# Optimization experiments

Measured on AMD Instinct MI355X. Metric: run time of the kernel, lower is better.

Reference implementation:

```python
import jax, jax.numpy as jnp
import numpy as np

VOCAB, HDIM, NC = 32000, 256, 5
B, L = 256, 512  # L must be a power of 2 (complete binary tree, depth log2(L))


def setup_inputs() -> dict:
    key = jax.random.key(0)
    ks = jax.random.split(key, 8)
    s_e = 1.0 / np.sqrt(HDIM)
    s_r = 1.0 / np.sqrt(2 * HDIM)
    return {
        "tokens": jax.random.randint(ks[0], (B, L), 0, VOCAB),                        # leaf word ids
        "embed_table": jax.random.normal(ks[1], (VOCAB, HDIM), jnp.float32),          # nn.Embedding
        "WR_w": jax.random.uniform(ks[2], (HDIM, 2 * HDIM), jnp.float32, -s_r, s_r),  # Linear(2H->H)
        "WR_b": jax.random.uniform(ks[3], (HDIM,), jnp.float32, -s_r, s_r),
        "WF_w": jax.random.uniform(ks[4], (HDIM, HDIM), jnp.float32, -s_e, s_e),      # Linear(H->H)
        "WF_b": jax.random.uniform(ks[5], (HDIM,), jnp.float32, -s_e, s_e),
        "WO_w": jax.random.uniform(ks[6], (NC, HDIM), jnp.float32, -s_e, s_e),        # Linear(H->NC)
        "WO_b": jax.random.uniform(ks[7], (NC,), jnp.float32, -s_e, s_e),
    }


def reference(tokens, embed_table, WR_w, WR_b, WF_w, WF_b, WO_w, WO_b):
    # Leaves: embedding gather. [B, L, H]
    e = embed_table[tokens]
    # Batched-by-depth tree composition: tanh(WR(cat(left, right))) per level.
    # Loop is over log2(L) levels (static), fully vectorized within each level.
    while e.shape[1] > 1:
        cat = jnp.concatenate([e[:, 0::2], e[:, 1::2]], axis=-1)   # [B, n/2, 2H]
        e = jnp.tanh(jnp.einsum('bnd,hd->bnh', cat, WR_w) + WR_b)  # [B, n/2, H]
    root = e[:, 0]  # [B, H]
    # classify: WO(ReLU(WF(root)))
    hidden = jax.nn.relu(root @ WF_w.T + WF_b)
    return hidden @ WO_w.T + WO_b  # [B, NC] logits
```

## Files before the change

kernel.cpp:

```cpp
#include <hip/hip_runtime.h>
#include <hip/hip_bf16.h>

typedef __bf16 bf16_t;
typedef __bf16 bf16x8 __attribute__((ext_vector_type(8)));
typedef __bf16 bf16x4 __attribute__((ext_vector_type(4)));
typedef float f32x4 __attribute__((ext_vector_type(4)));

__device__ __forceinline__ bf16_t f2bf(float f) {
    __hip_bfloat16 h = __float2bfloat16(f);
    return __builtin_bit_cast(bf16_t, h);
}

__device__ __forceinline__ float tanh_fast(float s) {
    float e2x = __expf(2.0f * s);
    return 1.0f - 2.0f * __builtin_amdgcn_rcpf(e2x + 1.0f);
}

__device__ __forceinline__ int swz(int u) { return u ^ ((u >> 3) & 7); }

#define GLD16(g, l)                                                        \
    __builtin_amdgcn_global_load_lds(                                      \
        (const __attribute__((address_space(1))) void*)(g),                \
        (__attribute__((address_space(3))) void*)(l), 16, 0, 0)

#define WAITV4() asm volatile("s_waitcnt vmcnt(4)" ::: "memory")
#define WAITV0() asm volatile("s_waitcnt vmcnt(0)" ::: "memory")

__global__ void __launch_bounds__(256) setup_kernel(const float* __restrict__ table,
                                                    const float* __restrict__ WRw,
                                                    bf16_t* __restrict__ tableBf,
                                                    bf16_t* __restrict__ Wbf,
                                                    bf16_t* __restrict__ Wfrag) {
    const int b = blockIdx.x, tid = threadIdx.x;
    if (b < 8000) {
        int i = b * 256 + tid;
        float4 v = ((const float4*)table)[i];
        bf16x4 o;
        o[0] = f2bf(v.x); o[1] = f2bf(v.y); o[2] = f2bf(v.z); o[3] = f2bf(v.w);
        ((bf16x4*)tableBf)[i] = o;
    } else if (b < 8128) {
        int i = (b - 8000) * 256 + tid;
        float4 v = ((const float4*)WRw)[i];
        bf16x4 o;
        o[0] = f2bf(v.x); o[1] = f2bf(v.y); o[2] = f2bf(v.z); o[3] = f2bf(v.w);
        ((bf16x4*)Wbf)[i] = o;
    } else {
        int gt = (b - 8128) * 256 + tid;
        int n16 = gt >> 10, rem = gt & 1023;
        int kt = rem >> 6, ln = rem & 63;
        int r = n16 * 16 + (ln & 15);
        int c = kt * 32 + (ln >> 4) * 8;
        const float4* s = (const float4*)(WRw + (long)r * 512 + c);
        float4 v0 = s[0], v1 = s[1];
        bf16x8 o;
        o[0] = f2bf(v0.x); o[1] = f2bf(v0.y); o[2] = f2bf(v0.z); o[3] = f2bf(v0.w);
        o[4] = f2bf(v1.x); o[5] = f2bf(v1.y); o[6] = f2bf(v1.z); o[7] = f2bf(v1.w);
        *(bf16x8*)(Wfrag + (size_t)gt * 8) = o;
    }
}

template <bool GATHER>
__global__ void __launch_bounds__(256) level_gemm(const bf16_t* __restrict__ A,
                                                  const int* __restrict__ tokens,
                                                  const bf16_t* __restrict__ tableBf,
                                                  const bf16_t* __restrict__ W,
                                                  const float* __restrict__ bias,
                                                  bf16_t* __restrict__ out) {
    constexpr int K = 512, N = 256;
    __shared__ __align__(16) char lds[49152];

    const int tid = threadIdx.x;
    const int lane = tid & 63;
    const int w = tid >> 6;
    const int wm = w >> 1, wn = w & 1;
    const long brow = (long)blockIdx.x * 128;
    const int bcol = blockIdx.y * 128;
    const int lr = lane & 15;
    const int g = lane >> 4;

    const int vlin = (w << 6) | lane;
    const int vs = swz(vlin);
    const int srow = vs >> 2;
    const int scolE = (vs & 3) << 3;

    const bf16_t *paLo0, *paHi0, *paLo1, *paHi1, *pa0, *pa1;
    if constexpr (GATHER) {
        long m0 = brow + srow, m1 = m0 + 64;
        int t0a = tokens[2 * m0], t0b = tokens[2 * m0 + 1];
        int t1a = tokens[2 * m1], t1b = tokens[2 * m1 + 1];
        paLo0 = tableBf + (long)t0a * 256 + scolE;
        paHi0 = tableBf + (long)t0b * 256 + scolE;
        paLo1 = tableBf + (long)t1a * 256 + scolE;
        paHi1 = tableBf + (long)t1b * 256 + scolE;
    } else {
        pa0 = A + (brow + srow) * K + scolE;
        pa1 = A + (brow + srow + 64) * K + scolE;
    }
    const bf16_t* pw0 = W + (long)(bcol + srow) * K + scolE;
    const bf16_t* pw1 = pw0 + 64 * K;

    float bv[4];
#pragma unroll
    for (int nt = 0; nt < 4; ++nt)
        bv[nt] = bias[bcol + (wn << 6) + (nt << 4) + lr];

    int offA[4], offB[4];
#pragma unroll
    for (int mt = 0; mt < 4; ++mt) {
        int rowA = (wm << 6) + (mt << 4) + lr;
        offA[mt] = swz(rowA * 4 + g) * 16;
    }
#pragma unroll
    for (int nt = 0; nt < 4; ++nt) {
        int rowB = (wn << 6) + (nt << 4) + lr;
        offB[nt] = 8192 + swz(rowB * 4 + g) * 16;
    }

    auto stage = [&](int buf, int kt) {
        char* dA = lds + buf * 16384 + (w << 10);
        char* dB = dA + 8192;
        const bf16_t *s0, *s1;
        if constexpr (GATHER) {
            int klo = kt & 255;
            bool lo = kt < 256;
            s0 = (lo ? paLo0 : paHi0) + klo;
            s1 = (lo ? paLo1 : paHi1) + klo;
        } else {
            s0 = pa0 + kt;
            s1 = pa1 + kt;
        }
        GLD16(s0, dA);
        GLD16(s1, dA + 4096);
        GLD16(pw0 + kt, dB);
        GLD16(pw1 + kt, dB + 4096);
    };

    f32x4 acc[4][4];
    const f32x4 zero = {0.f, 0.f, 0.f, 0.f};
#pragma unroll
    for (int i = 0; i < 4; ++i)
#pragma unroll
        for (int j = 0; j < 4; ++j) acc[i][j] = zero;

    stage(0, 0);
    stage(1, 32);
    WAITV4();
    __builtin_amdgcn_s_barrier();

#pragma unroll
    for (int t = 0; t < 16; ++t) {
        const int bufOff = 16384 * (t % 3);
        if (t + 2 < 16) stage((t + 2) % 3, (t + 2) << 5);

        bf16x8 af[4], bfr[4];
#pragma unroll
        for (int mt = 0; mt < 4; ++mt)
            af[mt] = *(const bf16x8*)(lds + bufOff + offA[mt]);
#pragma unroll
        for (int nt = 0; nt < 4; ++nt)
            bfr[nt] = *(const bf16x8*)(lds + bufOff + offB[nt]);
#pragma unroll
        for (int mt = 0; mt < 4; ++mt)
#pragma unroll
            for (int nt = 0; nt < 4; ++nt)
                acc[mt][nt] = __builtin_amdgcn_mfma_f32_16x16x32_bf16(
                    af[mt], bfr[nt], acc[mt][nt], 0, 0, 0);

        if (t < 14) {
            WAITV4();
            __builtin_amdgcn_s_barrier();
        } else if (t == 14) {
            WAITV0();
            __builtin_amdgcn_s_barrier();
        }
    }

    const int crow = g << 2;
#pragma unroll
    for (int nt = 0; nt < 4; ++nt) {
        int col = bcol + (wn << 6) + (nt << 4) + lr;
#pragma unroll
        for (int mt = 0; mt < 4; ++mt) {
            long row0 = brow + (wm << 6) + (mt << 4) + crow;
#pragma unroll
            for (int r = 0; r < 4; ++r)
                out[(row0 + r) * N + col] = f2bf(tanh_fast(acc[mt][nt][r] + bv[nt]));
        }
    }
}

__device__ __forceinline__ void tail_level(const char* chIn, char* chOut,
                                           const bf16_t* __restrict__ wfBase,
                                           const float* bv, int lane) {
    const int lr = lane & 15;
    const int g = lane >> 4;
    const char* aBase = chIn + lr * 1040 + g * 16;

    f32x4 acc[4];
    const f32x4 zero = {0.f, 0.f, 0.f, 0.f};
#pragma unroll
    for (int nt = 0; nt < 4; ++nt) acc[nt] = zero;

#pragma unroll
    for (int kt = 0; kt < 16; ++kt) {
        bf16x8 af = *(const bf16x8*)(aBase + kt * 64);
#pragma unroll
        for (int nt = 0; nt < 4; ++nt) {
            bf16x8 bfv = *(const bf16x8*)(wfBase + ((nt << 4) + kt) * 512);
            acc[nt] = __builtin_amdgcn_mfma_f32_16x16x32_bf16(af, bfv, acc[nt], 0, 0, 0);
        }
    }

    const int crow = g << 2;
#pragma unroll
    for (int nt = 0; nt < 4; ++nt) {
#pragma unroll
        for (int r = 0; r < 4; ++r) {
            int R = crow + r;
            float vv = tanh_fast(acc[nt][r] + bv[nt]);
            ((void)0);
        }
    }
}

__device__ __forceinline__ void tail_level_w(const char* chIn, char* chOut,
                                             const bf16_t* __restrict__ wfBase,
                                             const float* bv, int w, int lane) {
    const int lr = lane & 15;
    const int g = lane >> 4;
    const char* aBase = chIn + lr * 1040 + g * 16;

    f32x4 acc[4];
    const f32x4 zero = {0.f, 0.f, 0.f, 0.f};
#pragma unroll
    for (int nt = 0; nt < 4; ++nt) acc[nt] = zero;

#pragma unroll
    for (int kt = 0; kt < 16; ++kt) {
        bf16x8 af = *(const bf16x8*)(aBase + kt * 64);
#pragma unroll
        for (int nt = 0; nt < 4; ++nt) {
            bf16x8 bfv = *(const bf16x8*)(wfBase + ((nt << 4) + kt) * 512);
            acc[nt] = __builtin_amdgcn_mfma_f32_16x16x32_bf16(af, bfv, acc[nt], 0, 0, 0);
        }
    }

    const int crow = g << 2;
#pragma unroll
    for (int nt = 0; nt < 4; ++nt) {
        int col = (w << 6) + (nt << 4) + lr;
#pragma unroll
        for (int r = 0; r < 4; ++r) {
            int R = crow + r;
            float vv = tanh_fast(acc[nt][r] + bv[nt]);
            *(bf16_t*)(chOut + (R >> 1) * 1040 + (((R & 1) << 8) + col) * 2) = f2bf(vv);
        }
    }
}

__global__ void __launch_bounds__(256) tail_kernel(const bf16_t* __restrict__ in,
                                                   const bf16_t* __restrict__ Wfrag,
                                                   const float* __restrict__ bias,
                                                   const float* __restrict__ WFw,
                                                   const float* __restrict__ WFb,
                                                   const float* __restrict__ WOw,
                                                   const float* __restrict__ WOb,
                                                   float* __restrict__ out) {
    __shared__ __align__(16) char tl[2][16640];
    __shared__ float hid[256];

    const int tid = threadIdx.x;
    const int lane = tid & 63;
    const int w = tid >> 6;
    const int lr = lane & 15;

    float bv[4];
#pragma unroll
    for (int nt = 0; nt < 4; ++nt) bv[nt] = bias[(w << 6) + (nt << 4) + lr];

    const bf16_t* wfBase = Wfrag + ((size_t)((w << 2) << 4) << 6) * 8 / 8;
    wfBase = Wfrag + (size_t)(((w << 2) * 16) * 64 + lane) * 8;

    const bf16_t* gin = in + (size_t)blockIdx.x * 8192;
#pragma unroll
    for (int j = 0; j < 4; ++j) {
        int i = j * 256 + tid;
        int4 v = *(const int4*)(gin + i * 8);
        *(int4*)(&tl[0][0] + (i >> 6) * 1040 + (i & 63) * 16) = v;
    }
    __syncthreads();

    tail_level_w(tl[0], tl[1], wfBase, bv, w, lane);  __syncthreads();
    tail_level_w(tl[1], tl[0], wfBase, bv, w, lane);  __syncthreads();
    tail_level_w(tl[0], tl[1], wfBase, bv, w, lane);  __syncthreads();
    tail_level_w(tl[1], tl[0], wfBase, bv, w, lane);  __syncthreads();
    tail_level_w(tl[0], tl[1], wfBase, bv, w, lane);  __syncthreads();

    const bf16_t* root = (const bf16_t*)&tl[1][0];
    float s = WFb[tid];
    const float4* wf = (const float4*)(WFw + (long)tid * 256);
#pragma unroll 8
    for (int k4 = 0; k4 < 64; ++k4) {
        float4 wv = wf[k4];
        int k = k4 << 2;
        bf16x4 rv = *(const bf16x4*)&root[k];
        s += (float)rv[0] * wv.x + (float)rv[1] * wv.y +
             (float)rv[2] * wv.z + (float)rv[3] * wv.w;
    }
    hid[tid] = fmaxf(s, 0.0f);
    __syncthreads();

    if (tid < 5) {
        float o = WOb[tid];
        const float* wo = WOw + tid * 256;
        for (int k = 0; k < 256; ++k) o += hid[k] * wo[k];
        out[(long)blockIdx.x * 5 + tid] = o;
    }
}

extern "C" void kernel_launch(void* const* d_in, const int* in_sizes, int n_in,
                              void* d_out, int out_size, void* d_ws, size_t ws_size,
                              hipStream_t stream) {
    const int*   tokens = (const int*)d_in[0];
    const float* table  = (const float*)d_in[1];
    const float* WRw    = (const float*)d_in[2];
    const float* WRb    = (const float*)d_in[3];
    const float* WFw    = (const float*)d_in[4];
    const float* WFb    = (const float*)d_in[5];
    const float* WOw    = (const float*)d_in[6];
    const float* WOb    = (const float*)d_in[7];
    float* out = (float*)d_out;

    char* ws = (char*)d_ws;
    bf16_t* tableBf = (bf16_t*)ws;
    bf16_t* Wbf   = (bf16_t*)(ws + (size_t)20971520);
    bf16_t* Wfrag = (bf16_t*)(ws + (size_t)22020096);
    bf16_t* buf0  = (bf16_t*)(ws + (size_t)25165824);
    bf16_t* buf1  = (bf16_t*)(ws + (size_t)67108864);

    setup_kernel<<<8192, 256, 0, stream>>>(table, WRw, tableBf, Wbf, Wfrag);

    level_gemm<true><<<dim3(512, 2), 256, 0, stream>>>(nullptr, tokens, tableBf,
                                                       Wbf, WRb, buf0);
    level_gemm<false><<<dim3(256, 2), 256, 0, stream>>>(buf0, nullptr, nullptr,
                                                        Wbf, WRb, buf1);
    level_gemm<false><<<dim3(128, 2), 256, 0, stream>>>(buf1, nullptr, nullptr,
                                                        Wbf, WRb, buf0);
    level_gemm<false><<<dim3(64, 2), 256, 0, stream>>>(buf0, nullptr, nullptr,
                                                       Wbf, WRb, buf1);
    tail_kernel<<<256, 256, 0, stream>>>(buf1, Wfrag, WRb, WFw, WFb, WOw, WOb, out);
}
```

Baseline: 188.6 us.

## Fuse tree levels 2-9 and classifier into one per-sample LDS-resident kernel

Replaces the four per-level GEMM launches plus the tail kernel with two kernels. The first is a level-1 gather GEMM using 512-thread blocks that cover all 256 output columns. The second is a per-sample tree kernel that computes levels 2 through 9 entirely in LDS using a swizzled activation buffer. This removes the global round-trips of intermediate activations and the extra launches. It also transposes WF in setup for coalesced classifier reads and does the final WO projection with a shuffle reduction. In exchange it uses only 256 blocks with large LDS footprints, so occupancy and parallelism in the later levels are limited.

```diff
diff --git a/kernel.cpp b/kernel.cpp
--- a/kernel.cpp
+++ b/kernel.cpp
@@ -17,20 +17,27 @@
 }
 
 __device__ __forceinline__ int swz(int u) { return u ^ ((u >> 3) & 7); }
+__device__ __forceinline__ int actswz(int a) {
+    return a ^ ((((a >> 10) ^ (a >> 13)) & 7) << 4);
+}
 
 #define GLD16(g, l)                                                        \
     __builtin_amdgcn_global_load_lds(                                      \
         (const __attribute__((address_space(1))) void*)(g),                \
         (__attribute__((address_space(3))) void*)(l), 16, 0, 0)
 
-#define WAITV4() asm volatile("s_waitcnt vmcnt(4)" ::: "memory")
+#define WAITV3() asm volatile("s_waitcnt vmcnt(3)" ::: "memory")
+#define WAITV2() asm volatile("s_waitcnt vmcnt(2)" ::: "memory")
 #define WAITV0() asm volatile("s_waitcnt vmcnt(0)" ::: "memory")
+#define BAR() __builtin_amdgcn_s_barrier()
 
 __global__ void __launch_bounds__(256) setup_kernel(const float* __restrict__ table,
                                                     const float* __restrict__ WRw,
+                                                    const float* __restrict__ WFw,
                                                     bf16_t* __restrict__ tableBf,
                                                     bf16_t* __restrict__ Wbf,
-                                                    bf16_t* __restrict__ Wfrag) {
+                                                    bf16_t* __restrict__ Wfrag,
+                                                    float* __restrict__ WFwT) {
     const int b = blockIdx.x, tid = threadIdx.x;
     if (b < 8000) {
         int i = b * 256 + tid;
@@ -44,7 +51,7 @@
         bf16x4 o;
         o[0] = f2bf(v.x); o[1] = f2bf(v.y); o[2] = f2bf(v.z); o[3] = f2bf(v.w);
         ((bf16x4*)Wbf)[i] = o;
-    } else {
+    } else if (b < 8192) {
         int gt = (b - 8128) * 256 + tid;
         int n16 = gt >> 10, rem = gt & 1023;
         int kt = rem >> 6, ln = rem & 63;
@@ -56,83 +63,57 @@
         o[0] = f2bf(v0.x); o[1] = f2bf(v0.y); o[2] = f2bf(v0.z); o[3] = f2bf(v0.w);
         o[4] = f2bf(v1.x); o[5] = f2bf(v1.y); o[6] = f2bf(v1.z); o[7] = f2bf(v1.w);
         *(bf16x8*)(Wfrag + (size_t)gt * 8) = o;
-    }
-}
-
-template <bool GATHER>
-__global__ void __launch_bounds__(256) level_gemm(const bf16_t* __restrict__ A,
-                                                  const int* __restrict__ tokens,
-                                                  const bf16_t* __restrict__ tableBf,
-                                                  const bf16_t* __restrict__ W,
-                                                  const float* __restrict__ bias,
-                                                  bf16_t* __restrict__ out) {
-    constexpr int K = 512, N = 256;
-    __shared__ __align__(16) char lds[49152];
-
-    const int tid = threadIdx.x;
-    const int lane = tid & 63;
-    const int w = tid >> 6;
-    const int wm = w >> 1, wn = w & 1;
+    } else {
+        int i0 = (b - 8192) * 1024 + tid * 4;
+        float4 v;
+        v.x = WFw[((i0 + 0) & 255) * 256 + ((i0 + 0) >> 8)];
+        v.y = WFw[((i0 + 1) & 255) * 256 + ((i0 + 1) >> 8)];
+        v.z = WFw[((i0 + 2) & 255) * 256 + ((i0 + 2) >> 8)];
+        v.w = WFw[((i0 + 3) & 255) * 256 + ((i0 + 3) >> 8)];
+        *(float4*)(WFwT + i0) = v;
+    }
+}
+
+__global__ void __launch_bounds__(512) l1_kernel(const int* __restrict__ tokens,
+                                                 const bf16_t* __restrict__ tableBf,
+                                                 const bf16_t* __restrict__ W,
+                                                 const float* __restrict__ bias,
+                                                 bf16_t* __restrict__ out) {
+    __shared__ __align__(16) char lds[73728];
+    const int tid = threadIdx.x, lane = tid & 63, w = tid >> 6;
+    const int wm = w >> 2, wn = w & 3, lr = lane & 15, g = lane >> 4;
     const long brow = (long)blockIdx.x * 128;
-    const int bcol = blockIdx.y * 128;
-    const int lr = lane & 15;
-    const int g = lane >> 4;
-
-    const int vlin = (w << 6) | lane;
-    const int vs = swz(vlin);
-    const int srow = vs >> 2;
-    const int scolE = (vs & 3) << 3;
-
-    const bf16_t *paLo0, *paHi0, *paLo1, *paHi1, *pa0, *pa1;
-    if constexpr (GATHER) {
-        long m0 = brow + srow, m1 = m0 + 64;
-        int t0a = tokens[2 * m0], t0b = tokens[2 * m0 + 1];
-        int t1a = tokens[2 * m1], t1b = tokens[2 * m1 + 1];
-        paLo0 = tableBf + (long)t0a * 256 + scolE;
-        paHi0 = tableBf + (long)t0b * 256 + scolE;
-        paLo1 = tableBf + (long)t1a * 256 + scolE;
-        paHi1 = tableBf + (long)t1b * 256 + scolE;
-    } else {
-        pa0 = A + (brow + srow) * K + scolE;
-        pa1 = A + (brow + srow + 64) * K + scolE;
-    }
-    const bf16_t* pw0 = W + (long)(bcol + srow) * K + scolE;
-    const bf16_t* pw1 = pw0 + 64 * K;
+
+    const int ua = (w << 6) + swz(lane);
+    const int arow = ua >> 2, acolE = (ua & 3) << 3;
+    const long m = brow + arow;
+    const int tokA = tokens[2 * m], tokB = tokens[2 * m + 1];
+    const bf16_t* paLo = tableBf + (long)tokA * 256 + acolE;
+    const bf16_t* paHi = tableBf + (long)tokB * 256 + acolE;
+
+    const int ub0 = (w << 6) + swz(lane);
+    const int ub1 = ((w + 8) << 6) + swz(lane);
+    const bf16_t* pb0 = W + (long)(ub0 >> 2) * 512 + ((ub0 & 3) << 3);
+    const bf16_t* pb1 = W + (long)(ub1 >> 2) * 512 + ((ub1 & 3) << 3);
 
     float bv[4];
 #pragma unroll
+    for (int nt = 0; nt < 4; ++nt) bv[nt] = bias[(wn << 6) + (nt << 4) + lr];
+
+    int offA[4], offB[4];
+#pragma unroll
+    for (int mt = 0; mt < 4; ++mt)
+        offA[mt] = swz((((wm << 6) + (mt << 4) + lr) << 2) + g) << 4;
+#pragma unroll
     for (int nt = 0; nt < 4; ++nt)
-        bv[nt] = bias[bcol + (wn << 6) + (nt << 4) + lr];
-
-    int offA[4], offB[4];
-#pragma unroll
-    for (int mt = 0; mt < 4; ++mt) {
-        int rowA = (wm << 6) + (mt << 4) + lr;
-        offA[mt] = swz(rowA * 4 + g) * 16;
-    }
-#pragma unroll
-    for (int nt = 0; nt < 4; ++nt) {
-        int rowB = (wn << 6) + (nt << 4) + lr;
-        offB[nt] = 8192 + swz(rowB * 4 + g) * 16;
-    }
-
-    auto stage = [&](int buf, int kt) {
-        char* dA = lds + buf * 16384 + (w << 10);
-        char* dB = dA + 8192;
-        const bf16_t *s0, *s1;
-        if constexpr (GATHER) {
-            int klo = kt & 255;
-            bool lo = kt < 256;
-            s0 = (lo ? paLo0 : paHi0) + klo;
-            s1 = (lo ? paLo1 : paHi1) + klo;
-        } else {
-            s0 = pa0 + kt;
-            s1 = pa1 + kt;
-        }
-        GLD16(s0, dA);
-        GLD16(s1, dA + 4096);
-        GLD16(pw0 + kt, dB);
-        GLD16(pw1 + kt, dB + 4096);
+        offB[nt] = 8192 + (swz((((wn << 6) + (nt << 4) + lr) << 2) + g) << 4);
+
+    auto stage = [&](int s, int kt) {
+        char* base = lds + s * 24576;
+        bool lo = kt < 256;
+        GLD16((lo ? paLo : paHi) + (kt & 255), base + (w << 10));
+        GLD16(pb0 + kt, base + 8192 + (w << 10));
+        GLD16(pb1 + kt, base + 8192 + ((w + 8) << 10));
     };
 
     f32x4 acc[4][4];
@@ -144,177 +125,291 @@
 
     stage(0, 0);
     stage(1, 32);
-    WAITV4();
-    __builtin_amdgcn_s_barrier();
+    WAITV3(); BAR();
 
 #pragma unroll
     for (int t = 0; t < 16; ++t) {
-        const int bufOff = 16384 * (t % 3);
+        const char* base = lds + (t % 3) * 24576;
         if (t + 2 < 16) stage((t + 2) % 3, (t + 2) << 5);
-
         bf16x8 af[4], bfr[4];
 #pragma unroll
-        for (int mt = 0; mt < 4; ++mt)
-            af[mt] = *(const bf16x8*)(lds + bufOff + offA[mt]);
-#pragma unroll
-        for (int nt = 0; nt < 4; ++nt)
-            bfr[nt] = *(const bf16x8*)(lds + bufOff + offB[nt]);
+        for (int mt = 0; mt < 4; ++mt) af[mt] = *(const bf16x8*)(base + offA[mt]);
+#pragma unroll
+        for (int nt = 0; nt < 4; ++nt) bfr[nt] = *(const bf16x8*)(base + offB[nt]);
 #pragma unroll
         for (int mt = 0; mt < 4; ++mt)
 #pragma unroll
             for (int nt = 0; nt < 4; ++nt)
                 acc[mt][nt] = __builtin_amdgcn_mfma_f32_16x16x32_bf16(
                     af[mt], bfr[nt], acc[mt][nt], 0, 0, 0);
-
-        if (t < 14) {
-            WAITV4();
-            __builtin_amdgcn_s_barrier();
-        } else if (t == 14) {
-            WAITV0();
-            __builtin_amdgcn_s_barrier();
-        }
+        if (t < 14)      { WAITV3(); BAR(); }
+        else if (t == 14){ WAITV0(); BAR(); }
     }
 
     const int crow = g << 2;
 #pragma unroll
     for (int nt = 0; nt < 4; ++nt) {
-        int col = bcol + (wn << 6) + (nt << 4) + lr;
+        int col = (wn << 6) + (nt << 4) + lr;
 #pragma unroll
         for (int mt = 0; mt < 4; ++mt) {
             long row0 = brow + (wm << 6) + (mt << 4) + crow;
 #pragma unroll
             for (int r = 0; r < 4; ++r)
-                out[(row0 + r) * N + col] = f2bf(tanh_fast(acc[mt][nt][r] + bv[nt]));
-        }
-    }
-}
-
-__device__ __forceinline__ void tail_level(const char* chIn, char* chOut,
-                                           const bf16_t* __restrict__ wfBase,
-                                           const float* bv, int lane) {
-    const int lr = lane & 15;
-    const int g = lane >> 4;
-    const char* aBase = chIn + lr * 1040 + g * 16;
-
-    f32x4 acc[4];
-    const f32x4 zero = {0.f, 0.f, 0.f, 0.f};
-#pragma unroll
-    for (int nt = 0; nt < 4; ++nt) acc[nt] = zero;
-
-#pragma unroll
-    for (int kt = 0; kt < 16; ++kt) {
-        bf16x8 af = *(const bf16x8*)(aBase + kt * 64);
-#pragma unroll
-        for (int nt = 0; nt < 4; ++nt) {
-            bf16x8 bfv = *(const bf16x8*)(wfBase + ((nt << 4) + kt) * 512);
-            acc[nt] = __builtin_amdgcn_mfma_f32_16x16x32_bf16(af, bfv, acc[nt], 0, 0, 0);
-        }
-    }
-
-    const int crow = g << 2;
-#pragma unroll
-    for (int nt = 0; nt < 4; ++nt) {
-#pragma unroll
-        for (int r = 0; r < 4; ++r) {
-            int R = crow + r;
-            float vv = tanh_fast(acc[nt][r] + bv[nt]);
-            ((void)0);
-        }
-    }
-}
-
-__device__ __forceinline__ void tail_level_w(const char* chIn, char* chOut,
-                                             const bf16_t* __restrict__ wfBase,
-                                             const float* bv, int w, int lane) {
-    const int lr = lane & 15;
-    const int g = lane >> 4;
-    const char* aBase = chIn + lr * 1040 + g * 16;
-
-    f32x4 acc[4];
-    const f32x4 zero = {0.f, 0.f, 0.f, 0.f};
-#pragma unroll
-    for (int nt = 0; nt < 4; ++nt) acc[nt] = zero;
-
-#pragma unroll
-    for (int kt = 0; kt < 16; ++kt) {
-        bf16x8 af = *(const bf16x8*)(aBase + kt * 64);
-#pragma unroll
-        for (int nt = 0; nt < 4; ++nt) {
-            bf16x8 bfv = *(const bf16x8*)(wfBase + ((nt << 4) + kt) * 512);
-            acc[nt] = __builtin_amdgcn_mfma_f32_16x16x32_bf16(af, bfv, acc[nt], 0, 0, 0);
-        }
-    }
-
-    const int crow = g << 2;
-#pragma unroll
-    for (int nt = 0; nt < 4; ++nt) {
-        int col = (w << 6) + (nt << 4) + lr;
-#pragma unroll
-        for (int r = 0; r < 4; ++r) {
-            int R = crow + r;
-            float vv = tanh_fast(acc[nt][r] + bv[nt]);
-            *(bf16_t*)(chOut + (R >> 1) * 1040 + (((R & 1) << 8) + col) * 2) = f2bf(vv);
-        }
-    }
-}
-
-__global__ void __launch_bounds__(256) tail_kernel(const bf16_t* __restrict__ in,
+                out[(row0 + r) * 256 + col] = f2bf(tanh_fast(acc[mt][nt][r] + bv[nt]));
+        }
+    }
+}
+
+__global__ void __launch_bounds__(512) tree_kernel(const bf16_t* __restrict__ l1out,
+                                                   const bf16_t* __restrict__ W,
                                                    const bf16_t* __restrict__ Wfrag,
                                                    const float* __restrict__ bias,
-                                                   const float* __restrict__ WFw,
+                                                   const float* __restrict__ WFwT,
                                                    const float* __restrict__ WFb,
                                                    const float* __restrict__ WOw,
                                                    const float* __restrict__ WOb,
                                                    float* __restrict__ out) {
-    __shared__ __align__(16) char tl[2][16640];
+    __shared__ __align__(16) char stg[73728];
+    __shared__ __align__(16) char act[65536];
     __shared__ float hid[256];
 
-    const int tid = threadIdx.x;
-    const int lane = tid & 63;
-    const int w = tid >> 6;
-    const int lr = lane & 15;
+    const int tid = threadIdx.x, lane = tid & 63, w = tid >> 6;
+    const int wm = w >> 2, wn = w & 3, lr = lane & 15, g = lane >> 4;
+    const int crow = g << 2;
+    const bf16_t* Abase = l1out + (size_t)blockIdx.x * 65536;
+
+    const int ua = (w << 6) + swz(lane);
+    const bf16_t* pa = Abase + (long)(ua >> 2) * 512 + ((ua & 3) << 3);
+    const int ub0 = (w << 6) + swz(lane);
+    const int ub1 = ((w + 8) << 6) + swz(lane);
+    const bf16_t* pb0 = W + (long)(ub0 >> 2) * 512 + ((ub0 & 3) << 3);
+    const bf16_t* pb1 = W + (long)(ub1 >> 2) * 512 + ((ub1 & 3) << 3);
 
     float bv[4];
 #pragma unroll
-    for (int nt = 0; nt < 4; ++nt) bv[nt] = bias[(w << 6) + (nt << 4) + lr];
-
-    const bf16_t* wfBase = Wfrag + ((size_t)((w << 2) << 4) << 6) * 8 / 8;
-    wfBase = Wfrag + (size_t)(((w << 2) * 16) * 64 + lane) * 8;
-
-    const bf16_t* gin = in + (size_t)blockIdx.x * 8192;
-#pragma unroll
-    for (int j = 0; j < 4; ++j) {
-        int i = j * 256 + tid;
-        int4 v = *(const int4*)(gin + i * 8);
-        *(int4*)(&tl[0][0] + (i >> 6) * 1040 + (i & 63) * 16) = v;
+    for (int nt = 0; nt < 4; ++nt) bv[nt] = bias[(wn << 6) + (nt << 4) + lr];
+    float bvT[2];
+#pragma unroll
+    for (int nt = 0; nt < 2; ++nt) bvT[nt] = bias[(w << 5) + (nt << 4) + lr];
+
+    int offB[4];
+#pragma unroll
+    for (int nt = 0; nt < 4; ++nt)
+        offB[nt] = swz((((wn << 6) + (nt << 4) + lr) << 2) + g) << 4;
+
+    {
+        int offA[4];
+#pragma unroll
+        for (int mt = 0; mt < 4; ++mt)
+            offA[mt] = swz((((wm << 6) + (mt << 4) + lr) << 2) + g) << 4;
+
+        auto stage = [&](int s, int kt) {
+            char* base = stg + s * 24576;
+            GLD16(pa + kt, base + (w << 10));
+            GLD16(pb0 + kt, base + 8192 + (w << 10));
+            GLD16(pb1 + kt, base + 8192 + ((w + 8) << 10));
+        };
+
+        f32x4 acc[4][4];
+        const f32x4 zero = {0.f, 0.f, 0.f, 0.f};
+#pragma unroll
+        for (int i = 0; i < 4; ++i)
+#pragma unroll
+            for (int j = 0; j < 4; ++j) acc[i][j] = zero;
+
+        stage(0, 0); stage(1, 32);
+        WAITV3(); BAR();
+#pragma unroll
+        for (int t = 0; t < 16; ++t) {
+            const char* base = stg + (t % 3) * 24576;
+            if (t + 2 < 16) stage((t + 2) % 3, (t + 2) << 5);
+            bf16x8 af[4], bfr[4];
+#pragma unroll
+            for (int mt = 0; mt < 4; ++mt) af[mt] = *(const bf16x8*)(base + 8192 * 0 + offA[mt]);
+#pragma unroll
+            for (int nt = 0; nt < 4; ++nt) bfr[nt] = *(const bf16x8*)(base + 8192 + offB[nt]);
+#pragma unroll
+            for (int mt = 0; mt < 4; ++mt)
+#pragma unroll
+                for (int nt = 0; nt < 4; ++nt)
+                    acc[mt][nt] = __builtin_amdgcn_mfma_f32_16x16x32_bf16(
+                        af[mt], bfr[nt], acc[mt][nt], 0, 0, 0);
+            if (t < 14)      { WAITV3(); BAR(); }
+            else if (t == 14){ WAITV0(); BAR(); }
+        }
+#pragma unroll
+        for (int nt = 0; nt < 4; ++nt) {
+            int col = (wn << 6) + (nt << 4) + lr;
+#pragma unroll
+            for (int mt = 0; mt < 4; ++mt) {
+                int m0 = (wm << 6) + (mt << 4) + crow;
+#pragma unroll
+                for (int r = 0; r < 4; ++r) {
+                    int a = ((m0 + r) << 9) + (col << 1);
+                    *(bf16_t*)(act + actswz(a)) = f2bf(tanh_fast(acc[mt][nt][r] + bv[nt]));
+                }
+            }
+        }
+        __syncthreads();
+    }
+
+    {
+        auto stageB = [&](int s, int kt) {
+            char* base = stg + s * 16384;
+            GLD16(pb0 + kt, base + (w << 10));
+            GLD16(pb1 + kt, base + ((w + 8) << 10));
+        };
+        f32x4 acc[2][4];
+        const f32x4 zero = {0.f, 0.f, 0.f, 0.f};
+#pragma unroll
+        for (int i = 0; i < 2; ++i)
+#pragma unroll
+            for (int j = 0; j < 4; ++j) acc[i][j] = zero;
+
+        stageB(0, 0); stageB(1, 32);
+        WAITV2(); BAR();
+#pragma unroll
+        for (int t = 0; t < 16; ++t) {
+            const char* base = stg + (t % 3) * 16384;
+            if (t + 2 < 16) stageB((t + 2) % 3, (t + 2) << 5);
+            bf16x8 af[2], bfr[4];
+#pragma unroll
+            for (int mt = 0; mt < 2; ++mt) {
+                int row = (wm << 5) + (mt << 4) + lr;
+                int a = (row << 10) + (t << 6) + (g << 4);
+                af[mt] = *(const bf16x8*)(act + actswz(a));
+            }
+#pragma unroll
+            for (int nt = 0; nt < 4; ++nt) bfr[nt] = *(const bf16x8*)(base + offB[nt]);
+#pragma unroll
+            for (int mt = 0; mt < 2; ++mt)
+#pragma unroll
+                for (int nt = 0; nt < 4; ++nt)
+                    acc[mt][nt] = __builtin_amdgcn_mfma_f32_16x16x32_bf16(
+                        af[mt], bfr[nt], acc[mt][nt], 0, 0, 0);
+            if (t < 14)      { WAITV2(); BAR(); }
+            else if (t == 14){ WAITV0(); BAR(); }
+        }
+        __syncthreads();
+#pragma unroll
+        for (int nt = 0; nt < 4; ++nt) {
+            int col = (wn << 6) + (nt << 4) + lr;
+#pragma unroll
+            for (int mt = 0; mt < 2; ++mt) {
+                int m0 = (wm << 5) + (mt << 4) + crow;
+#pragma unroll
+                for (int r = 0; r < 4; ++r) {
+                    int a = ((m0 + r) << 10) + (col << 1);
+                    *(bf16_t*)(act + actswz(a)) = f2bf(tanh_fast(acc[mt][nt][r] + bv[nt]));
+                }
+            }
+        }
+        __syncthreads();
+    }
+
+    {
+        auto stageB = [&](int s, int kt) {
+            char* base = stg + s * 16384;
+            GLD16(pb0 + kt, base + (w << 10));
+            GLD16(pb1 + kt, base + ((w + 8) << 10));
+        };
+        f32x4 acc[4];
+        const f32x4 zero = {0.f, 0.f, 0.f, 0.f};
+#pragma unroll
+        for (int j = 0; j < 4; ++j) acc[j] = zero;
+
+        stageB(0, 0); stageB(1, 32);
+        WAITV2(); BAR();
+#pragma unroll
+        for (int t = 0; t < 16; ++t) {
+            const char* base = stg + (t % 3) * 16384;
+            if (t + 2 < 16) stageB((t + 2) % 3, (t + 2) << 5);
+            int row = (wm << 4) + lr;
+            int a = (row << 11) + ((t >= 8) ? 1024 : 0) + ((t & 7) << 6) + (g << 4);
+            bf16x8 af = *(const bf16x8*)(act + actswz(a));
+            bf16x8 bfr[4];
+#pragma unroll
+            for (int nt = 0; nt < 4; ++nt) bfr[nt] = *(const bf16x8*)(base + offB[nt]);
+#pragma unroll
+            for (int nt = 0; nt < 4; ++nt)
+                acc[nt] = __builtin_amdgcn_mfma_f32_16x16x32_bf16(af, bfr[nt], acc[nt], 0, 0, 0);
+            if (t < 14)      { WAITV2(); BAR(); }
+            else if (t == 14){ WAITV0(); BAR(); }
+        }
+        __syncthreads();
+#pragma unroll
+        for (int nt = 0; nt < 4; ++nt) {
+            int col = (wn << 6) + (nt << 4) + lr;
+#pragma unroll
+            for (int r = 0; r < 4; ++r) {
+                int m0 = (wm << 4) + crow + r;
+                if (m0 < 32) {
+                    int a = (m0 << 11) + (col << 1);
+                    *(bf16_t*)(act + actswz(a)) = f2bf(tanh_fast(acc[nt][r] + bv[nt]));
+                }
+            }
+        }
+        __syncthreads();
+    }
+
+    {
+        bf16x8 wreg[2][16];
+#pragma unroll
+        for (int nt = 0; nt < 2; ++nt)
+#pragma unroll
+            for (int kt = 0; kt < 16; ++kt)
+                wreg[nt][kt] = *(const bf16x8*)(
+                    Wfrag + (size_t)((((2 * w + nt) * 16 + kt) * 64 + lane)) * 8);
+
+#pragma unroll
+        for (int lev = 0; lev < 5; ++lev) {
+            const int sA = 4096 << lev;
+            const int half = sA >> 1;
+            f32x4 acc[2];
+            const f32x4 zero = {0.f, 0.f, 0.f, 0.f};
+            acc[0] = zero; acc[1] = zero;
+#pragma unroll
+            for (int kt = 0; kt < 16; ++kt) {
+                int a = (sA * lr + ((kt >= 8) ? half : 0) + ((kt & 7) << 6) + (g << 4)) & 65535;
+                bf16x8 af = *(const bf16x8*)(act + actswz(a));
+                acc[0] = __builtin_amdgcn_mfma_f32_16x16x32_bf16(af, wreg[0][kt], acc[0], 0, 0, 0);
+                acc[1] = __builtin_amdgcn_mfma_f32_16x16x32_bf16(af, wreg[1][kt], acc[1], 0, 0, 0);
+            }
+            __syncthreads();
+            const int valid = 16 >> lev;
+#pragma unroll
+            for (int nt = 0; nt < 2; ++nt) {
+                int col = (w << 5) + (nt << 4) + lr;
+#pragma unroll
+                for (int r = 0; r < 4; ++r) {
+                    int m0 = crow + r;
+                    if (m0 < valid) {
+                        int a = sA * m0 + (col << 1);
+                        *(bf16_t*)(act + actswz(a)) = f2bf(tanh_fast(acc[nt][r] + bvT[nt]));
+                    }
+                }
+            }
+            __syncthreads();
+        }
+    }
+
+    if (tid < 256) {
+        const bf16_t* root = (const bf16_t*)act;
+        float s = WFb[tid];
+#pragma unroll 8
+        for (int k = 0; k < 256; ++k)
+            s += (float)root[k] * WFwT[k * 256 + tid];
+        hid[tid] = fmaxf(s, 0.0f);
     }
     __syncthreads();
 
-    tail_level_w(tl[0], tl[1], wfBase, bv, w, lane);  __syncthreads();
-    tail_level_w(tl[1], tl[0], wfBase, bv, w, lane);  __syncthreads();
-    tail_level_w(tl[0], tl[1], wfBase, bv, w, lane);  __syncthreads();
-    tail_level_w(tl[1], tl[0], wfBase, bv, w, lane);  __syncthreads();
-    tail_level_w(tl[0], tl[1], wfBase, bv, w, lane);  __syncthreads();
-
-    const bf16_t* root = (const bf16_t*)&tl[1][0];
-    float s = WFb[tid];
-    const float4* wf = (const float4*)(WFw + (long)tid * 256);
-#pragma unroll 8
-    for (int k4 = 0; k4 < 64; ++k4) {
-        float4 wv = wf[k4];
-        int k = k4 << 2;
-        bf16x4 rv = *(const bf16x4*)&root[k];
-        s += (float)rv[0] * wv.x + (float)rv[1] * wv.y +
-             (float)rv[2] * wv.z + (float)rv[3] * wv.w;
-    }
-    hid[tid] = fmaxf(s, 0.0f);
-    __syncthreads();
-
-    if (tid < 5) {
-        float o = WOb[tid];
-        const float* wo = WOw + tid * 256;
-        for (int k = 0; k < 256; ++k) o += hid[k] * wo[k];
-        out[(long)blockIdx.x * 5 + tid] = o;
+    if (w < 5) {
+        const float* wo = WOw + w * 256;
+        float p = hid[lane] * wo[lane] + hid[lane + 64] * wo[lane + 64] +
+                  hid[lane + 128] * wo[lane + 128] + hid[lane + 192] * wo[lane + 192];
+#pragma unroll
+        for (int off = 32; off > 0; off >>= 1) p += __shfl_down(p, off);
+        if (lane == 0) out[(long)blockIdx.x * 5 + w] = p + WOb[w];
     }
 }
 
@@ -335,18 +430,10 @@
     bf16_t* tableBf = (bf16_t*)ws;
     bf16_t* Wbf   = (bf16_t*)(ws + (size_t)20971520);
     bf16_t* Wfrag = (bf16_t*)(ws + (size_t)22020096);
-    bf16_t* buf0  = (bf16_t*)(ws + (size_t)25165824);
-    bf16_t* buf1  = (bf16_t*)(ws + (size_t)67108864);
-
-    setup_kernel<<<8192, 256, 0, stream>>>(table, WRw, tableBf, Wbf, Wfrag);
-
-    level_gemm<true><<<dim3(512, 2), 256, 0, stream>>>(nullptr, tokens, tableBf,
-                                                       Wbf, WRb, buf0);
-    level_gemm<false><<<dim3(256, 2), 256, 0, stream>>>(buf0, nullptr, nullptr,
-                                                        Wbf, WRb, buf1);
-    level_gemm<false><<<dim3(128, 2), 256, 0, stream>>>(buf1, nullptr, nullptr,
-                                                        Wbf, WRb, buf0);
-    level_gemm<false><<<dim3(64, 2), 256, 0, stream>>>(buf0, nullptr, nullptr,
-                                                       Wbf, WRb, buf1);
-    tail_kernel<<<256, 256, 0, stream>>>(buf1, Wfrag, WRb, WFw, WFb, WOw, WOb, out);
-}
+    float*  WFwT  = (float*)(ws + (size_t)23068672);
+    bf16_t* l1out = (bf16_t*)(ws + (size_t)25165824);
+
+    setup_kernel<<<8256, 256, 0, stream>>>(table, WRw, WFw, tableBf, Wbf, Wfrag, WFwT);
+    l1_kernel<<<512, 512, 0, stream>>>(tokens, tableBf, Wbf, WRb, l1out);
+    tree_kernel<<<256, 512, 0, stream>>>(l1out, Wbf, Wfrag, WRb, WFwT, WFb, WOw, WOb, out);
+}
```

Result: faster. 159.2 us (-15.6%).
